# Optimization experiments

Hardware: AMD Instinct MI355X
Metric: run time of the kernel (lower is better)

The kernel has to match this reference:

```python
import jax, jax.numpy as jnp
import numpy as np

N, E, F_IN, H, C, ED, NODES = 25000, 100000, 16, 4, 280, 6, 6


def setup_inputs() -> dict:
    key = jax.random.key(0)
    ks = jax.random.split(key, 16)
    s = lambda k, sh: jax.random.normal(k, sh, dtype=jnp.float32) * 0.05
    return {
        "x": jax.random.normal(ks[0], (N, F_IN), dtype=jnp.float32),
        "edge_index": jax.random.randint(ks[1], (2, E), 0, N, dtype=jnp.int64),
        "edge_attr": jax.random.normal(ks[2], (E, ED), dtype=jnp.float32),
        # TransformerConv params (PyG): lin_query/key/value (bias), lin_edge (no bias), lin_skip (bias)
        "Wq": s(ks[3], (F_IN, H * C)), "bq": jnp.zeros((H * C,), jnp.float32),
        "Wk": s(ks[4], (F_IN, H * C)), "bk": jnp.zeros((H * C,), jnp.float32),
        "Wv": s(ks[5], (F_IN, H * C)), "bv": jnp.zeros((H * C,), jnp.float32),
        "We": s(ks[6], (ED, H * C)),
        "Wskip": s(ks[7], (F_IN, C)), "bskip": jnp.zeros((C,), jnp.float32),
        # MLP: 280 -> 64 -> 16 -> NODES, softmax
        "W1": s(ks[8], (280, 64)), "b1": jnp.zeros((64,), jnp.float32),
        "W2": s(ks[9], (64, 16)), "b2": jnp.zeros((16,), jnp.float32),
        "W3": s(ks[10], (16, NODES)), "b3": jnp.zeros((NODES,), jnp.float32),
    }


def reference(x, edge_index, edge_attr, Wq, bq, Wk, bk, Wv, bv, We, Wskip, bskip, W1, b1, W2, b2, W3, b3):
    n = x.shape[0]
    src, dst = edge_index[0], edge_index[1]  # message j -> i (PyG convention)
    q = (x @ Wq + bq).reshape(n, H, C)
    k = (x @ Wk + bk).reshape(n, H, C)
    v = (x @ Wv + bv).reshape(n, H, C)
    e = (edge_attr @ We).reshape(-1, H, C)  # [E,H,C]
    kj = k[src] + e                          # gather + edge features
    alpha = jnp.einsum('ehc,ehc->eh', q[dst], kj) / jnp.sqrt(jnp.float32(C))  # [E,H]
    # numerically stable segment softmax over destination nodes
    amax = jax.ops.segment_max(alpha, dst, num_segments=n)
    ex = jnp.exp(alpha - amax[dst])
    denom = jax.ops.segment_sum(ex, dst, num_segments=n)
    attn = ex / (denom[dst] + 1e-16)
    out = jax.ops.segment_sum(attn[..., None] * (v[src] + e), dst, num_segments=n)  # [N,H,C]
    out = out.mean(axis=1)                  # concat=False -> mean over heads
    out = out + x @ Wskip + bskip           # root/skip connection
    h = out.reshape(-1, 280)
    h = jax.nn.relu(h @ W1 + b1)
    h = jax.nn.relu(h @ W2 + b2)
    return jax.nn.softmax(h @ W3 + b3, axis=-1)
```

## Files before the change

kernel.cpp:

```cpp
#include <hip/hip_runtime.h>

#define N_NODES 25000
#define N_EDGES 100000
#define CH 280
#define HC 1120
#define CAP 32

typedef unsigned int uint;
typedef unsigned short ushort;
typedef __attribute__((ext_vector_type(8))) short short8;
typedef __attribute__((ext_vector_type(4))) float f32x4;

#define FAC_A 0
#define FAC_B 1024
#define FAC_C 1408
#define FAC_D 1472
#define FAC_F 1536
#define FAC_G 1560
#define FAC_TOTAL 1564

#define WC_K 128

#define P_FAC_END  25
#define P_WC_END   57
#define P_W2_END   58
#define P_TOTAL    449

__device__ __forceinline__ ushort f2bf(float f) {
  union { float f; uint u; } c; c.f = f;
  uint u = c.u + 0x7FFFu + ((c.u >> 16) & 1u);
  return (ushort)(u >> 16);
}

__global__ __launch_bounds__(256) void prep_kernel(
    const float* __restrict__ Wq, const float* __restrict__ Wk,
    const float* __restrict__ We, const float* __restrict__ bq,
    const float* __restrict__ bk, float* __restrict__ fac,
    const float* __restrict__ Wv, const float* __restrict__ bv,
    const float* __restrict__ Wskip, const float* __restrict__ bskip,
    const float* __restrict__ W1, const float* __restrict__ b1,
    ushort* __restrict__ Wct,
    const float* __restrict__ W2, ushort* __restrict__ W2tg,
    const int* __restrict__ ei, const float* __restrict__ ea,
    int* __restrict__ cursor, float* __restrict__ erec) {
  int b = blockIdx.x;
  int tid = threadIdx.x;
  if (b < P_FAC_END) {
    int t4 = b * 256 + tid;
    int q = t4 >> 2, li = t4 & 3;
    if (q >= FAC_TOTAL) return;
    const float *pa, *pb;
    if (q < FAC_B) {
      int h = q >> 8, f = (q >> 4) & 15, g = q & 15;
      pa = Wq + f * HC + h * CH; pb = Wk + g * HC + h * CH;
    } else if (q < FAC_C) {
      int u = q - FAC_B; int h = u / 96, v2 = u % 96, f = v2 / 6, j = v2 % 6;
      pa = Wq + f * HC + h * CH; pb = We + j * HC + h * CH;
    } else if (q < FAC_D) {
      int u = q - FAC_C; int h = u >> 4, f = u & 15;
      pa = Wq + f * HC + h * CH; pb = bk + h * CH;
    } else if (q < FAC_F) {
      int u = q - FAC_D; int h = u >> 4, g = u & 15;
      pa = Wk + g * HC + h * CH; pb = bq + h * CH;
    } else if (q < FAC_G) {
      int u = q - FAC_F; int h = u / 6, j = u % 6;
      pa = We + j * HC + h * CH; pb = bq + h * CH;
    } else {
      int h = q - FAC_G;
      pa = bq + h * CH; pb = bk + h * CH;
    }
    float acc = 0.f;
    int c0 = li * 70;
    for (int c = c0; c < c0 + 70; ++c) acc = fmaf(pa[c], pb[c], acc);
    acc += __shfl_xor(acc, 1);
    acc += __shfl_xor(acc, 2);
    if (li == 0) fac[q] = acc;
  } else if (b < P_WC_END) {
    int wid = tid >> 6;
    int r = __builtin_amdgcn_readfirstlane((b - P_FAC_END) * 4 + wid);
    int k = tid & 63;
    float v = 0.f;
    bool wz = true;
    if (r < 113) {
      const float* w = nullptr;
      float scale = 1.f;
      bool zero = false;
      if (r < 96) {
        int h = r / 24, j = r % 24;
        if (j == 23) zero = true;
        else {
          if (j < 16) w = Wv + j * HC + h * CH;
          else if (j < 22) w = We + (j - 16) * HC + h * CH;
          else w = bv + h * CH;
          scale = 0.25f;
        }
      } else if (r < 112) {
        w = Wskip + (r - 96) * CH;
      } else {
        w = bskip;
      }
      if (!zero) {
        float acc = 0.f;
        for (int c = 0; c < CH; ++c) acc = fmaf(w[c], W1[c * 64 + k], acc);
        v = acc * scale;
        if (r == 112) v += b1[k];
        wz = false;
      }
    }
    Wct[k * WC_K + r] = wz ? (ushort)0 : f2bf(v);
  } else if (b < P_W2_END) {
    for (int t = tid; t < 1024; t += 256) {
      int m2 = t >> 6, k = t & 63;
      W2tg[m2 * 64 + k] = f2bf(W2[(size_t)k * 16 + m2]);
    }
  } else {
    int e = (b - P_W2_END) * 256 + tid;
    if (e >= N_EDGES) return;
    int src = ei[e];
    int dst = ei[N_EDGES + e];
    int pos = atomicAdd(&cursor[dst], 1);
    if (pos >= CAP) return;
    const float2* s2 = (const float2*)(ea + (size_t)e * 6);
    float2 e01 = s2[0], e23 = s2[1], e45 = s2[2];
    int4 w0;
    w0.x = src;
    w0.y = __float_as_int(e01.x); w0.z = __float_as_int(e01.y);
    w0.w = __float_as_int(e23.x);
    float4 w1 = make_float4(e23.y, e45.x, e45.y, 0.f);
    float* dstp = erec + ((size_t)dst * CAP + pos) * 8;
    *(int4*)dstp = w0;
    *(float4*)(dstp + 4) = w1;
  }
}

__global__ __launch_bounds__(256, 2) void fused_kernel(
    const float* __restrict__ x, const float* __restrict__ fac,
    const float* __restrict__ erec, const int* __restrict__ cursor,
    const ushort* __restrict__ Wct, const ushort* __restrict__ W2tg,
    const float* __restrict__ b2, const float* __restrict__ W3,
    const float* __restrict__ b3, float* __restrict__ out) {
  __shared__ ushort Vls[64 * 136];
  __shared__ ushort Wcs[64 * 136];
  __shared__ ushort W2ts[16 * 72];
  __shared__ ushort h1b[64 * 72];
  __shared__ float  h2s[64 * 17];
  const float RS = 0.05976143046671968f;
  int tid = threadIdx.x;
  int wid = tid >> 6, lane = tid & 63;
  int h = __builtin_amdgcn_readfirstlane(wid);

  {
    int row = tid >> 2, seg = tid & 3;
    const ushort* src = Wct + row * 128 + seg * 32;
    ushort* dst = Wcs + row * 136 + seg * 32;
#pragma unroll
    for (int i = 0; i < 4; ++i)
      *(int4*)(dst + i * 8) = *(const int4*)(src + i * 8);
  }
  if (tid < 128) {
    int row = tid >> 3, seg = tid & 7;
    *(int4*)(W2ts + row * 72 + seg * 8) = *(const int4*)(W2tg + row * 64 + seg * 8);
  }

  int n0 = blockIdx.x * 64 + lane;
  bool valid = n0 < N_NODES;
  int n = valid ? n0 : (N_NODES - 1);
  float xv[16];
  {
    const float4* x4 = (const float4*)(x + (size_t)n * 16);
#pragma unroll
    for (int i = 0; i < 4; ++i) {
      float4 q = x4[i];
      xv[4 * i] = q.x; xv[4 * i + 1] = q.y; xv[4 * i + 2] = q.z; xv[4 * i + 3] = q.w;
    }
  }
  const float* Af = fac + FAC_A + h * 256;
  const float* Bf = fac + FAC_B + h * 96;
  const float* cf = fac + FAC_C + h * 16;
  const float* df = fac + FAC_D + h * 16;
  const float* ff = fac + FAC_F + h * 6;
  const float  gf = fac[FAC_G + h];
  float va[16];
#pragma unroll
  for (int g = 0; g < 16; ++g) {
    float a = df[g];
#pragma unroll
    for (int f = 0; f < 16; ++f) a = fmaf(xv[f], Af[f * 16 + g], a);
    va[g] = a;
  }
  float ve[6];
#pragma unroll
  for (int j = 0; j < 6; ++j) {
    float a = ff[j];
#pragma unroll
    for (int f = 0; f < 16; ++f) a = fmaf(xv[f], Bf[f * 6 + j], a);
    ve[j] = a;
  }
  float v22 = gf;
#pragma unroll
  for (int f = 0; f < 16; ++f) v22 = fmaf(xv[f], cf[f], v22);

  int dg = valid ? cursor[n0] : 0;
  if (dg > CAP) dg = CAP;
  float m = -1e30f, den = 0.f;
  float Sx[16];
  float Sa[6];
#pragma unroll
  for (int f = 0; f < 16; ++f) Sx[f] = 0.f;
#pragma unroll
  for (int j = 0; j < 6; ++j) Sa[j] = 0.f;
  for (int q2 = 0; q2 < dg; ++q2) {
    const float* er = erec + ((size_t)n0 * CAP + q2) * 8;
    int4 ra = *(const int4*)er;
    float4 rb = *(const float4*)(er + 4);
    int s = ra.x;
    const float4* xs4 = (const float4*)(x + (size_t)s * 16);
    float4 a0 = xs4[0], a1 = xs4[1], a2 = xs4[2], a3 = xs4[3];
    float xs[16] = {a0.x, a0.y, a0.z, a0.w, a1.x, a1.y, a1.z, a1.w,
                    a2.x, a2.y, a2.z, a2.w, a3.x, a3.y, a3.z, a3.w};
    float eav[6] = {__int_as_float(ra.y), __int_as_float(ra.z),
                    __int_as_float(ra.w), rb.x, rb.y, rb.z};
    float alpha = v22;
#pragma unroll
    for (int f = 0; f < 16; ++f) alpha = fmaf(va[f], xs[f], alpha);
#pragma unroll
    for (int j = 0; j < 6; ++j) alpha = fmaf(ve[j], eav[j], alpha);
    alpha *= RS;
    float nm = fmaxf(m, alpha);
    float sc = __expf(m - nm);
    float w = __expf(alpha - nm);
    den = den * sc + w;
#pragma unroll
    for (int f = 0; f < 16; ++f) Sx[f] = fmaf(Sx[f], sc, w * xs[f]);
#pragma unroll
    for (int j = 0; j < 6; ++j) Sa[j] = fmaf(Sa[j], sc, w * eav[j]);
    m = nm;
  }
  {
    float inv = 1.f / (den + 1e-16f);
    float outv[24];
#pragma unroll
    for (int f = 0; f < 16; ++f) outv[f] = Sx[f] * inv;
#pragma unroll
    for (int j = 0; j < 6; ++j) outv[16 + j] = Sa[j] * inv;
    outv[22] = den * inv;
    outv[23] = 0.f;
    uint pk[12];
#pragma unroll
    for (int i = 0; i < 12; ++i)
      pk[i] = (uint)f2bf(outv[2 * i]) | ((uint)f2bf(outv[2 * i + 1]) << 16);
    int4* vp = (int4*)(Vls + lane * 136 + h * 24);
    int4 s0, s1, s2;
    s0.x = (int)pk[0]; s0.y = (int)pk[1]; s0.z = (int)pk[2]; s0.w = (int)pk[3];
    s1.x = (int)pk[4]; s1.y = (int)pk[5]; s1.z = (int)pk[6]; s1.w = (int)pk[7];
    s2.x = (int)pk[8]; s2.y = (int)pk[9]; s2.z = (int)pk[10]; s2.w = (int)pk[11];
    vp[0] = s0; vp[1] = s1; vp[2] = s2;
  }
  if (wid == 0) {
    uint pk[8];
#pragma unroll
    for (int i = 0; i < 8; ++i)
      pk[i] = (uint)f2bf(xv[2 * i]) | ((uint)f2bf(xv[2 * i + 1]) << 16);
    int4* vp = (int4*)(Vls + lane * 136 + 96);
    int4 s0, s1, s2, s3;
    s0.x = (int)pk[0]; s0.y = (int)pk[1]; s0.z = (int)pk[2]; s0.w = (int)pk[3];
    s1.x = (int)pk[4]; s1.y = (int)pk[5]; s1.z = (int)pk[6]; s1.w = (int)pk[7];
    s2.x = (int)0x3F80u; s2.y = 0; s2.z = 0; s2.w = 0;
    s3.x = 0; s3.y = 0; s3.z = 0; s3.w = 0;
    vp[0] = s0; vp[1] = s1; vp[2] = s2; vp[3] = s3;
  }
  __syncthreads();

  int col15 = lane & 15, quad = lane >> 4;
  f32x4 acc[4];
#pragma unroll
  for (int T = 0; T < 4; ++T) acc[T] = (f32x4){0.f, 0.f, 0.f, 0.f};
#pragma unroll
  for (int kk = 0; kk < 4; ++kk) {
    int k0 = kk * 32;
    short8 a = *(const short8*)(Vls + (wid * 16 + col15) * 136 + k0 + quad * 8);
#pragma unroll
    for (int T = 0; T < 4; ++T) {
      short8 bfr = *(const short8*)(Wcs + (T * 16 + col15) * 136 + k0 + quad * 8);
      acc[T] = __builtin_amdgcn_mfma_f32_16x16x32_bf16(a, bfr, acc[T], 0, 0, 0);
    }
  }
#pragma unroll
  for (int T = 0; T < 4; ++T) {
#pragma unroll
    for (int r = 0; r < 4; ++r) {
      int nloc = wid * 16 + quad * 4 + r;
      int c = T * 16 + col15;
      h1b[nloc * 72 + c] = f2bf(fmaxf(acc[T][r], 0.f));
    }
  }
  __syncthreads();
  float b2v = b2[col15];
  f32x4 acc2 = (f32x4){0.f, 0.f, 0.f, 0.f};
#pragma unroll
  for (int kk = 0; kk < 2; ++kk) {
    int k0 = kk * 32;
    short8 a2 = *(const short8*)(h1b + (wid * 16 + col15) * 72 + k0 + quad * 8);
    short8 bf2 = *(const short8*)(W2ts + col15 * 72 + k0 + quad * 8);
    acc2 = __builtin_amdgcn_mfma_f32_16x16x32_bf16(a2, bf2, acc2, 0, 0, 0);
  }
#pragma unroll
  for (int r = 0; r < 4; ++r) {
    int nloc = wid * 16 + quad * 4 + r;
    h2s[nloc * 17 + col15] = fmaxf(acc2[r] + b2v, 0.f);
  }
  __syncthreads();
  if (tid < 64) {
    int n2 = blockIdx.x * 64 + tid;
    if (n2 < N_NODES) {
      float hv[16];
#pragma unroll
      for (int j = 0; j < 16; ++j) hv[j] = h2s[tid * 17 + j];
      float lg[6];
      float mx = -1e30f;
#pragma unroll
      for (int o = 0; o < 6; ++o) {
        float a = b3[o];
#pragma unroll
        for (int j = 0; j < 16; ++j) a = fmaf(hv[j], W3[j * 6 + o], a);
        lg[o] = a; mx = fmaxf(mx, a);
      }
      float s = 0.f;
#pragma unroll
      for (int o = 0; o < 6; ++o) { lg[o] = __expf(lg[o] - mx); s += lg[o]; }
      float inv = 1.f / s;
      float2* o2 = (float2*)(out + (size_t)n2 * 6);
      o2[0] = make_float2(lg[0] * inv, lg[1] * inv);
      o2[1] = make_float2(lg[2] * inv, lg[3] * inv);
      o2[2] = make_float2(lg[4] * inv, lg[5] * inv);
    }
  }
}

extern "C" void kernel_launch(void* const* d_in, const int* in_sizes, int n_in,
                              void* d_out, int out_size, void* d_ws, size_t ws_size,
                              hipStream_t stream) {
  const float* x     = (const float*)d_in[0];
  const int*   ei    = (const int*)d_in[1];
  const float* ea    = (const float*)d_in[2];
  const float* Wq    = (const float*)d_in[3];
  const float* bq    = (const float*)d_in[4];
  const float* Wk    = (const float*)d_in[5];
  const float* bk    = (const float*)d_in[6];
  const float* Wv    = (const float*)d_in[7];
  const float* bv    = (const float*)d_in[8];
  const float* We    = (const float*)d_in[9];
  const float* Wskip = (const float*)d_in[10];
  const float* bskip = (const float*)d_in[11];
  const float* W1    = (const float*)d_in[12];
  const float* b1    = (const float*)d_in[13];
  const float* W2    = (const float*)d_in[14];
  const float* b2    = (const float*)d_in[15];
  const float* W3    = (const float*)d_in[16];
  const float* b3    = (const float*)d_in[17];
  float* out = (float*)d_out;
  (void)in_sizes; (void)n_in; (void)out_size; (void)ws_size;

  char* ws = (char*)d_ws;
  size_t off = 0;
  auto alloc = [&](size_t bytes) {
    void* p = ws + off;
    off = (off + bytes + 255) & ~(size_t)255;
    return p;
  };
  float*  fac    = (float*)alloc(FAC_TOTAL * 4);
  ushort* Wct    = (ushort*)alloc(64 * WC_K * 2);
  int*    cursor = (int*)alloc(N_NODES * 4);
  ushort* W2tg   = (ushort*)alloc(16 * 64 * 2);
  float*  erec   = (float*)alloc((size_t)N_NODES * CAP * 8 * 4);

  hipMemsetAsync(cursor, 0, N_NODES * 4, stream);
  prep_kernel<<<P_TOTAL, 256, 0, stream>>>(
      Wq, Wk, We, bq, bk, fac, Wv, bv, Wskip, bskip, W1, b1, Wct, W2, W2tg,
      ei, ea, cursor, erec);
  fused_kernel<<<391, 256, 0, stream>>>(x, fac, erec, cursor, Wct, W2tg,
                                        b2, W3, b3, out);
}
```

Baseline: 118.1 us.

## Store compact slot-major edge records and process two edges per iteration with prefetch

The prep pass now writes an 8-byte (src, edge id) record per edge into a slot-major array indexed by pos*N+dst, instead of a 32-byte node-major record that copied the edge attributes. The fused kernel reads these records with coalesced accesses across neighbouring nodes, gathers edge attributes straight from the input, prefetches the next pair of records, and folds two edges into each online-softmax update. This cuts scatter write traffic and improves record-load coalescing. In exchange it adds a dependent gather on edge_attr and uses more registers for the two-edge body.

```diff
diff --git a/kernel.cpp b/kernel.cpp
--- a/kernel.cpp
+++ b/kernel.cpp
@@ -41,8 +41,8 @@
     const float* __restrict__ W1, const float* __restrict__ b1,
     ushort* __restrict__ Wct,
     const float* __restrict__ W2, ushort* __restrict__ W2tg,
-    const int* __restrict__ ei, const float* __restrict__ ea,
-    int* __restrict__ cursor, float* __restrict__ erec) {
+    const int* __restrict__ ei,
+    int* __restrict__ cursor, int2* __restrict__ erec) {
   int b = blockIdx.x;
   int tid = threadIdx.x;
   if (b < P_FAC_END) {
@@ -120,22 +120,14 @@
     int dst = ei[N_EDGES + e];
     int pos = atomicAdd(&cursor[dst], 1);
     if (pos >= CAP) return;
-    const float2* s2 = (const float2*)(ea + (size_t)e * 6);
-    float2 e01 = s2[0], e23 = s2[1], e45 = s2[2];
-    int4 w0;
-    w0.x = src;
-    w0.y = __float_as_int(e01.x); w0.z = __float_as_int(e01.y);
-    w0.w = __float_as_int(e23.x);
-    float4 w1 = make_float4(e23.y, e45.x, e45.y, 0.f);
-    float* dstp = erec + ((size_t)dst * CAP + pos) * 8;
-    *(int4*)dstp = w0;
-    *(float4*)(dstp + 4) = w1;
+    erec[(size_t)pos * N_NODES + dst] = make_int2(src, e);
   }
 }
 
 __global__ __launch_bounds__(256, 2) void fused_kernel(
-    const float* __restrict__ x, const float* __restrict__ fac,
-    const float* __restrict__ erec, const int* __restrict__ cursor,
+    const float* __restrict__ x, const float* __restrict__ ea,
+    const float* __restrict__ fac,
+    const int2* __restrict__ erec, const int* __restrict__ cursor,
     const ushort* __restrict__ Wct, const ushort* __restrict__ W2tg,
     const float* __restrict__ b2, const float* __restrict__ W3,
     const float* __restrict__ b3, float* __restrict__ out) {
@@ -209,32 +201,57 @@
   for (int f = 0; f < 16; ++f) Sx[f] = 0.f;
 #pragma unroll
   for (int j = 0; j < 6; ++j) Sa[j] = 0.f;
-  for (int q2 = 0; q2 < dg; ++q2) {
-    const float* er = erec + ((size_t)n0 * CAP + q2) * 8;
-    int4 ra = *(const int4*)er;
-    float4 rb = *(const float4*)(er + 4);
-    int s = ra.x;
-    const float4* xs4 = (const float4*)(x + (size_t)s * 16);
-    float4 a0 = xs4[0], a1 = xs4[1], a2 = xs4[2], a3 = xs4[3];
-    float xs[16] = {a0.x, a0.y, a0.z, a0.w, a1.x, a1.y, a1.z, a1.w,
-                    a2.x, a2.y, a2.z, a2.w, a3.x, a3.y, a3.z, a3.w};
-    float eav[6] = {__int_as_float(ra.y), __int_as_float(ra.z),
-                    __int_as_float(ra.w), rb.x, rb.y, rb.z};
-    float alpha = v22;
-#pragma unroll
-    for (int f = 0; f < 16; ++f) alpha = fmaf(va[f], xs[f], alpha);
-#pragma unroll
-    for (int j = 0; j < 6; ++j) alpha = fmaf(ve[j], eav[j], alpha);
-    alpha *= RS;
-    float nm = fmaxf(m, alpha);
-    float sc = __expf(m - nm);
-    float w = __expf(alpha - nm);
-    den = den * sc + w;
-#pragma unroll
-    for (int f = 0; f < 16; ++f) Sx[f] = fmaf(Sx[f], sc, w * xs[f]);
-#pragma unroll
-    for (int j = 0; j < 6; ++j) Sa[j] = fmaf(Sa[j], sc, w * eav[j]);
-    m = nm;
+  if (dg > 0) {
+    int2 r0 = erec[n0];
+    int2 r1 = (dg > 1) ? erec[N_NODES + n0] : r0;
+    for (int q2 = 0; q2 < dg; q2 += 2) {
+      int2 p0 = r0, p1 = r1;
+      if (q2 + 2 < dg) {
+        p0 = erec[(size_t)(q2 + 2) * N_NODES + n0];
+        p1 = (q2 + 3 < dg) ? erec[(size_t)(q2 + 3) * N_NODES + n0] : p0;
+      }
+      bool has1 = (q2 + 1 < dg);
+      const float4* xa = (const float4*)(x + (size_t)r0.x * 16);
+      float4 a0 = xa[0], a1 = xa[1], a2 = xa[2], a3 = xa[3];
+      const float2* eap = (const float2*)(ea + (size_t)r0.y * 6);
+      float2 e0 = eap[0], e1 = eap[1], e2 = eap[2];
+      const float4* xb = (const float4*)(x + (size_t)r1.x * 16);
+      float4 b0v = xb[0], b1v = xb[1], b2v = xb[2], b3v = xb[3];
+      const float2* ebp = (const float2*)(ea + (size_t)r1.y * 6);
+      float2 f0 = ebp[0], f1 = ebp[1], f2 = ebp[2];
+      float xs0[16] = {a0.x, a0.y, a0.z, a0.w, a1.x, a1.y, a1.z, a1.w,
+                       a2.x, a2.y, a2.z, a2.w, a3.x, a3.y, a3.z, a3.w};
+      float ev0[6] = {e0.x, e0.y, e1.x, e1.y, e2.x, e2.y};
+      float xs1[16] = {b0v.x, b0v.y, b0v.z, b0v.w, b1v.x, b1v.y, b1v.z, b1v.w,
+                       b2v.x, b2v.y, b2v.z, b2v.w, b3v.x, b3v.y, b3v.z, b3v.w};
+      float ev1[6] = {f0.x, f0.y, f1.x, f1.y, f2.x, f2.y};
+      float al0 = v22, al1 = v22;
+#pragma unroll
+      for (int f = 0; f < 16; ++f) {
+        al0 = fmaf(va[f], xs0[f], al0);
+        al1 = fmaf(va[f], xs1[f], al1);
+      }
+#pragma unroll
+      for (int j = 0; j < 6; ++j) {
+        al0 = fmaf(ve[j], ev0[j], al0);
+        al1 = fmaf(ve[j], ev1[j], al1);
+      }
+      al0 *= RS; al1 *= RS;
+      if (!has1) al1 = -1e30f;
+      float nm = fmaxf(m, fmaxf(al0, al1));
+      float sc = __expf(m - nm);
+      float w0 = __expf(al0 - nm);
+      float w1 = __expf(al1 - nm);
+      den = den * sc + w0 + w1;
+#pragma unroll
+      for (int f = 0; f < 16; ++f)
+        Sx[f] = fmaf(Sx[f], sc, fmaf(w0, xs0[f], w1 * xs1[f]));
+#pragma unroll
+      for (int j = 0; j < 6; ++j)
+        Sa[j] = fmaf(Sa[j], sc, fmaf(w0, ev0[j], w1 * ev1[j]));
+      m = nm;
+      r0 = p0; r1 = p1;
+    }
   }
   {
     float inv = 1.f / (den + 1e-16f);
@@ -372,12 +389,12 @@
   ushort* Wct    = (ushort*)alloc(64 * WC_K * 2);
   int*    cursor = (int*)alloc(N_NODES * 4);
   ushort* W2tg   = (ushort*)alloc(16 * 64 * 2);
-  float*  erec   = (float*)alloc((size_t)N_NODES * CAP * 8 * 4);
+  int2*   erec   = (int2*)alloc((size_t)CAP * N_NODES * 8);
 
   hipMemsetAsync(cursor, 0, N_NODES * 4, stream);
   prep_kernel<<<P_TOTAL, 256, 0, stream>>>(
       Wq, Wk, We, bq, bk, fac, Wv, bv, Wskip, bskip, W1, b1, Wct, W2, W2tg,
-      ei, ea, cursor, erec);
-  fused_kernel<<<391, 256, 0, stream>>>(x, fac, erec, cursor, Wct, W2tg,
+      ei, cursor, erec);
+  fused_kernel<<<391, 256, 0, stream>>>(x, ea, fac, erec, cursor, Wct, W2tg,
                                         b2, W3, b3, out);
 }
```

Measured after the change: 119.9 us. Within noise of the previous version (+1.5%).
